# Kernel optimization log

Hardware: AMD Instinct MI355X
Metric: run time of the kernel (lower is better)

The kernel has to match this reference:

```python
import jax, jax.numpy as jnp
import numpy as np

B = 256       # decode batch
V = 50257     # per-model vocab size (GPT-2-class)
U = 65536     # union vocab size
M = 3         # number of ensembled models


def setup_inputs() -> dict:
    key = jax.random.key(0)
    ks = jax.random.split(key, 7)
    d = {}
    for i in range(M):
        d[f"logits{i}"] = jax.random.normal(ks[i], (B, V), dtype=jnp.float32)
    for i in range(M):
        # vocab_to_token_id mapping: model-local vocab index -> union vocab index
        d[f"map{i}"] = jax.random.randint(ks[M + i], (V,), 0, U, dtype=jnp.int32)
    d["weights"] = jnp.array([0.4, 0.35, 0.25], dtype=jnp.float32)
    return d


def reference(logits0, logits1, logits2, map0, map1, map2, weights):
    # union_probs[b, map_m[j]] += w_m * softmax(logits_m)[b, j]
    union = jnp.zeros((logits0.shape[0], U), dtype=logits0.dtype)
    for m, (lg, mp) in enumerate(zip((logits0, logits1, logits2),
                                     (map0, map1, map2))):
        p = jax.nn.softmax(lg, axis=-1)          # [B, V]
        union = union.at[:, mp].add(weights[m] * p)  # weighted scatter-add into [B, U]
    return union
```

## Files before the change

### kernel.cpp

```cpp
#include <hip/hip_runtime.h>

#define BB 256
#define VV 50257
#define UU 65536
#define MM 3
#define NT 1024

typedef float float4a __attribute__((ext_vector_type(4), aligned(4)));

#define WS_WINV   0
#define WS_HIST   3072
#define WS_OFF    7168
#define WS_CURSOR 11296
#define WS_SORTED 15392
#define WS_ET     618496
#define WS_NEED   77813248ull

__global__ __launch_bounds__(512) void row_sums_kernel(
    const float* __restrict__ l0, const float* __restrict__ l1,
    const float* __restrict__ l2, const float* __restrict__ weights,
    float* __restrict__ winv)
{
    const int bx = blockIdx.x;
    const int m  = bx >> 8;
    const int b  = bx & 255;
    const float* lg  = (m == 0) ? l0 : (m == 1) ? l1 : l2;
    const float* row = lg + (size_t)b * VV;
    const float4a* rowv = (const float4a*)row;

    const int nv4 = VV / 4;
    float partial = 0.0f;
    for (int i = threadIdx.x; i < nv4; i += 512) {
        float4a v = rowv[i];
        partial += __expf(v.x) + __expf(v.y) + __expf(v.z) + __expf(v.w);
    }
    if (threadIdx.x == 0) partial += __expf(row[VV - 1]);

    #pragma unroll
    for (int off = 32; off > 0; off >>= 1)
        partial += __shfl_down(partial, off, 64);

    __shared__ float smem[8];
    const int lane = threadIdx.x & 63;
    const int wv   = threadIdx.x >> 6;
    if (lane == 0) smem[wv] = partial;
    __syncthreads();
    if (threadIdx.x == 0) {
        float tot = 0.0f;
        #pragma unroll
        for (int w = 0; w < 8; ++w) tot += smem[w];
        winv[bx] = weights[m] / tot;
    }
}

__global__ __launch_bounds__(1024) void hist_count_kernel(
    const int* __restrict__ m0, const int* __restrict__ m1,
    const int* __restrict__ m2, int* __restrict__ hist)
{
    __shared__ int h[NT];
    for (int i = threadIdx.x; i < NT; i += 1024) h[i] = 0;
    __syncthreads();
    const int total = MM * VV;
    for (int idx = blockIdx.x * 1024 + threadIdx.x; idx < total;
         idx += gridDim.x * 1024) {
        const int m = idx / VV;
        const int j = idx - m * VV;
        const int* mp = (m == 0) ? m0 : (m == 1) ? m1 : m2;
        atomicAdd(&h[mp[j] >> 6], 1);
    }
    __syncthreads();
    for (int i = threadIdx.x; i < NT; i += 1024) atomicAdd(&hist[i], h[i]);
}

__global__ __launch_bounds__(1024) void prefix_kernel(
    const int* __restrict__ hist, int* __restrict__ off, int* __restrict__ cursor)
{
    __shared__ int s[NT];
    const int t = threadIdx.x;
    const int mine = hist[t];
    s[t] = mine;
    __syncthreads();
    for (int d = 1; d < NT; d <<= 1) {
        int v = (t >= d) ? s[t - d] : 0;
        __syncthreads();
        s[t] += v;
        __syncthreads();
    }
    const int excl = s[t] - mine;
    off[t] = excl;
    cursor[t] = excl;
    if (t == NT - 1) off[NT] = s[t];
}

__global__ __launch_bounds__(256) void sort_kernel(
    const int* __restrict__ m0, const int* __restrict__ m1,
    const int* __restrict__ m2, int* __restrict__ cursor,
    int* __restrict__ sorted)
{
    const int total = MM * VV;
    for (int idx = blockIdx.x * 256 + threadIdx.x; idx < total;
         idx += gridDim.x * 256) {
        const int m = idx / VV;
        const int j = idx - m * VV;
        const int* mp = (m == 0) ? m0 : (m == 1) ? m1 : m2;
        const int u = mp[j];
        const int pos = atomicAdd(&cursor[u >> 6], 1);
        sorted[pos] = (j << 8) | (m << 6) | (u & 63);
    }
}

__global__ __launch_bounds__(256) void transpose_exp_kernel(
    const float* __restrict__ l0, const float* __restrict__ l1,
    const float* __restrict__ l2, _Float16* __restrict__ ET)
{
    const int m  = blockIdx.z;
    const float* lg = (m == 0) ? l0 : (m == 1) ? l1 : l2;
    const int j0 = blockIdx.x * 64;
    const int b0 = blockIdx.y * 64;
    __shared__ float tile[64][65];
    const int lane = threadIdx.x & 63;
    const int sub  = threadIdx.x >> 6;

    const int j = j0 + lane;
    if (j < VV) {
        #pragma unroll
        for (int rr = 0; rr < 16; ++rr) {
            const int b = b0 + rr * 4 + sub;
            tile[lane][rr * 4 + sub] = __expf(lg[(size_t)b * VV + j]);
        }
    }
    __syncthreads();
    #pragma unroll
    for (int rr = 0; rr < 16; ++rr) {
        const int jj = rr * 4 + sub;
        const int jw = j0 + jj;
        if (jw < VV)
            ET[((size_t)m * VV + jw) * BB + b0 + lane] = (_Float16)tile[jj][lane];
    }
}

__global__ __launch_bounds__(256) void accumulate_kernel(
    const _Float16* __restrict__ ET, const int* __restrict__ sorted,
    const int* __restrict__ off, const float* __restrict__ winv,
    float* __restrict__ out)
{
    const int k = blockIdx.x;
    const int t = threadIdx.x;

    __shared__ float acc[64 * 256];
    for (int i = t; i < 64 * 256; i += 256) acc[i] = 0.0f;
    const float w0 = winv[0 * BB + t];
    const float w1 = winv[1 * BB + t];
    const float w2 = winv[2 * BB + t];
    __syncthreads();

    const int s = off[k], e = off[k + 1];
    #pragma unroll 4
    for (int i = s; i < e; ++i) {
        const int pack = sorted[i];
        const int ul = pack & 63;
        const int m  = (pack >> 6) & 3;
        const int j  = pack >> 8;
        const float ev = (float)ET[((size_t)m * VV + j) * BB + t];
        const float w  = (m == 0) ? w0 : (m == 1) ? w1 : w2;
        acc[ul * 256 + (t ^ (ul & 31))] += w * ev;
    }
    __syncthreads();

    const int u0 = k * 64;
    const int lane = t & 63, sub = t >> 6;
    #pragma unroll 4
    for (int c = 0; c < 64; ++c) {
        const int b = sub + c * 4;
        out[(size_t)b * UU + u0 + lane] = acc[lane * 256 + (b ^ (lane & 31))];
    }
}

#define FB_NBUCK 8
#define FB_BSZ   8192

__global__ __launch_bounds__(256) void fb_count_kernel(
    const int* __restrict__ m0, const int* __restrict__ m1,
    const int* __restrict__ m2, int* __restrict__ cnt)
{
    const int m = blockIdx.y;
    const int* mp = (m == 0) ? m0 : (m == 1) ? m1 : m2;
    __shared__ int hist[FB_NBUCK];
    if (threadIdx.x < FB_NBUCK) hist[threadIdx.x] = 0;
    __syncthreads();
    const int j = blockIdx.x * 256 + threadIdx.x;
    if (j < VV) atomicAdd(&hist[mp[j] >> 13], 1);
    __syncthreads();
    if (threadIdx.x < FB_NBUCK)
        atomicAdd(&cnt[m * FB_NBUCK + threadIdx.x], hist[threadIdx.x]);
}

__global__ void fb_prefix_kernel(const int* __restrict__ cnt,
                                 int* __restrict__ off, int* __restrict__ cursor)
{
    for (int m = 0; m < MM; ++m) {
        int acc = 0;
        for (int k = 0; k < FB_NBUCK; ++k) {
            off[m * (FB_NBUCK + 1) + k] = acc;
            cursor[m * FB_NBUCK + k]    = acc;
            acc += cnt[m * FB_NBUCK + k];
        }
        off[m * (FB_NBUCK + 1) + FB_NBUCK] = acc;
    }
}

__global__ __launch_bounds__(256) void fb_scatter_kernel(
    const int* __restrict__ m0, const int* __restrict__ m1,
    const int* __restrict__ m2, int* __restrict__ cursor,
    int* __restrict__ sorted)
{
    const int m = blockIdx.y;
    const int* mp = (m == 0) ? m0 : (m == 1) ? m1 : m2;
    int* srt = sorted + (size_t)m * VV;
    const int j = blockIdx.x * 256 + threadIdx.x;
    int u = 0, bucket = FB_NBUCK;
    if (j < VV) { u = mp[j]; bucket = u >> 13; }
    const int lane = threadIdx.x & 63;
    const unsigned long long lt = (1ull << lane) - 1ull;
    #pragma unroll
    for (int k = 0; k < FB_NBUCK; ++k) {
        unsigned long long mask = __ballot(bucket == k);
        if (mask) {
            int leader = __ffsll((long long)mask) - 1;
            int base = 0;
            if (lane == leader)
                base = atomicAdd(&cursor[m * FB_NBUCK + k], __popcll(mask));
            base = __shfl(base, leader, 64);
            if (bucket == k) {
                int pos = base + __popcll(mask & lt);
                srt[pos] = ((u & (FB_BSZ - 1)) << 16) | j;
            }
        }
    }
}

__global__ __launch_bounds__(512) void fb_accumulate_kernel(
    const float* __restrict__ l0, const float* __restrict__ l1,
    const float* __restrict__ l2,
    const int* __restrict__ sorted, const int* __restrict__ off,
    const float* __restrict__ winv, float* __restrict__ out)
{
    const int k = blockIdx.x;
    const int b = blockIdx.y;
    __shared__ float acc[FB_BSZ];
    for (int i = threadIdx.x; i < FB_BSZ; i += 512) acc[i] = 0.0f;
    __syncthreads();
    #pragma unroll
    for (int m = 0; m < MM; ++m) {
        const float* lg = (m == 0) ? l0 : (m == 1) ? l1 : l2;
        const float* row = lg + (size_t)b * VV;
        const int* srt = sorted + (size_t)m * VV;
        const float wv = winv[m * BB + b];
        const int s = off[m * (FB_NBUCK + 1) + k];
        const int e = off[m * (FB_NBUCK + 1) + k + 1];
        for (int i = s + threadIdx.x; i < e; i += 512) {
            const int pack = srt[i];
            atomicAdd(&acc[pack >> 16], wv * __expf(row[pack & 0xFFFF]));
        }
    }
    __syncthreads();
    float* orow = out + (size_t)b * UU + (size_t)k * FB_BSZ;
    for (int i = threadIdx.x; i < FB_BSZ; i += 512) orow[i] = acc[i];
}

extern "C" void kernel_launch(void* const* d_in, const int* in_sizes, int n_in,
                              void* d_out, int out_size, void* d_ws, size_t ws_size,
                              hipStream_t stream)
{
    const float* l0 = (const float*)d_in[0];
    const float* l1 = (const float*)d_in[1];
    const float* l2 = (const float*)d_in[2];
    const int*   m0 = (const int*)d_in[3];
    const int*   m1 = (const int*)d_in[4];
    const int*   m2 = (const int*)d_in[5];
    const float* w  = (const float*)d_in[6];
    float* out = (float*)d_out;
    char* ws = (char*)d_ws;

    if (ws_size >= WS_NEED) {
        float*    winv   = (float*)   (ws + WS_WINV);
        int*      hist   = (int*)     (ws + WS_HIST);
        int*      off    = (int*)     (ws + WS_OFF);
        int*      cursor = (int*)     (ws + WS_CURSOR);
        int*      sorted = (int*)     (ws + WS_SORTED);
        _Float16* ET     = (_Float16*)(ws + WS_ET);

        hipMemsetAsync(hist, 0, NT * sizeof(int), stream);

        row_sums_kernel<<<MM * BB, 512, 0, stream>>>(l0, l1, l2, w, winv);
        hist_count_kernel<<<64, 1024, 0, stream>>>(m0, m1, m2, hist);
        prefix_kernel<<<1, 1024, 0, stream>>>(hist, off, cursor);
        sort_kernel<<<256, 256, 0, stream>>>(m0, m1, m2, cursor, sorted);

        dim3 gtr((VV + 63) / 64, BB / 64, MM);
        transpose_exp_kernel<<<gtr, 256, 0, stream>>>(l0, l1, l2, ET);

        accumulate_kernel<<<NT, 256, 0, stream>>>(ET, sorted, off, winv, out);
    } else {
        float* winv   = (float*)(ws + 0);
        int*   cnt    = (int*)  (ws + 3072);
        int*   off    = (int*)  (ws + 3200);
        int*   cursor = (int*)  (ws + 3456);
        int*   sorted = (int*)  (ws + 3584);

        hipMemsetAsync(cnt, 0, MM * FB_NBUCK * sizeof(int), stream);
        row_sums_kernel<<<MM * BB, 512, 0, stream>>>(l0, l1, l2, w, winv);
        dim3 gmap((VV + 255) / 256, MM);
        fb_count_kernel<<<gmap, 256, 0, stream>>>(m0, m1, m2, cnt);
        fb_prefix_kernel<<<1, 1, 0, stream>>>(cnt, off, cursor);
        fb_scatter_kernel<<<gmap, 256, 0, stream>>>(m0, m1, m2, cursor, sorted);
        dim3 gacc(FB_NBUCK, BB);
        fb_accumulate_kernel<<<gacc, 512, 0, stream>>>(l0, l1, l2, sorted, off, winv, out);
    }
}
```

Baseline: 339.1 us.

## Fuse row sums into transpose-exp kernel and split accumulate across two warp groups

The separate row-sum pass over the logits is dropped. The transpose-exp kernel now loops over 8 column tiles per block and accumulates per-row partial sums of exp, which a small kernel reduces into the inverse weights. This removes one full read of the logits and one exp pass. The accumulate kernel now uses 512 threads, with two groups splitting the sorted entries and using shared-memory atomics, which raises parallelism at the cost of atomic overhead. The partials buffer reuses the sorted region, which is safe only because winv_kernel consumes the partials before sort_kernel overwrites them.

```diff
diff --git a/kernel.cpp b/kernel.cpp
--- a/kernel.cpp
+++ b/kernel.cpp
@@ -5,6 +5,8 @@
 #define UU 65536
 #define MM 3
 #define NT 1024
+#define NJT 786
+#define NJC 99
 
 typedef float float4a __attribute__((ext_vector_type(4), aligned(4)));
 
@@ -16,41 +18,66 @@
 #define WS_ET     618496
 #define WS_NEED   77813248ull
 
-__global__ __launch_bounds__(512) void row_sums_kernel(
+__global__ __launch_bounds__(256) void transpose_exp_sum_kernel(
     const float* __restrict__ l0, const float* __restrict__ l1,
-    const float* __restrict__ l2, const float* __restrict__ weights,
+    const float* __restrict__ l2, _Float16* __restrict__ ET,
+    float* __restrict__ partials)
+{
+    const int m  = blockIdx.z;
+    const float* lg = (m == 0) ? l0 : (m == 1) ? l1 : l2;
+    const int b0 = blockIdx.y * 64;
+    const int jc = blockIdx.x;
+    const int lane = threadIdx.x & 63;
+    const int sub  = threadIdx.x >> 6;
+
+    __shared__ float tile[64][65];
+    __shared__ float psum[4][64];
+    float fsum = 0.0f;
+
+    for (int tt = 0; tt < 8; ++tt) {
+        const int jt = jc * 8 + tt;
+        if (jt >= NJT) break;
+        const int j0 = jt * 64;
+        const int j  = j0 + lane;
+        if (j < VV) {
+            #pragma unroll
+            for (int rr = 0; rr < 16; ++rr) {
+                const int b = b0 + rr * 4 + sub;
+                tile[lane][rr * 4 + sub] = __expf(lg[(size_t)b * VV + j]);
+            }
+        }
+        __syncthreads();
+        #pragma unroll
+        for (int rr = 0; rr < 16; ++rr) {
+            const int jj = rr * 4 + sub;
+            const int jw = j0 + jj;
+            if (jw < VV) {
+                const float v = tile[jj][lane];
+                ET[((size_t)m * VV + jw) * BB + b0 + lane] = (_Float16)v;
+                fsum += v;
+            }
+        }
+        __syncthreads();
+    }
+    psum[sub][lane] = fsum;
+    __syncthreads();
+    if (threadIdx.x < 64) {
+        const float tot = psum[0][threadIdx.x] + psum[1][threadIdx.x]
+                        + psum[2][threadIdx.x] + psum[3][threadIdx.x];
+        partials[((m << 8) + b0 + threadIdx.x) * NJC + jc] = tot;
+    }
+}
+
+__global__ __launch_bounds__(64) void winv_kernel(
+    const float* __restrict__ partials, const float* __restrict__ weights,
     float* __restrict__ winv)
 {
-    const int bx = blockIdx.x;
-    const int m  = bx >> 8;
-    const int b  = bx & 255;
-    const float* lg  = (m == 0) ? l0 : (m == 1) ? l1 : l2;
-    const float* row = lg + (size_t)b * VV;
-    const float4a* rowv = (const float4a*)row;
-
-    const int nv4 = VV / 4;
-    float partial = 0.0f;
-    for (int i = threadIdx.x; i < nv4; i += 512) {
-        float4a v = rowv[i];
-        partial += __expf(v.x) + __expf(v.y) + __expf(v.z) + __expf(v.w);
-    }
-    if (threadIdx.x == 0) partial += __expf(row[VV - 1]);
-
-    #pragma unroll
-    for (int off = 32; off > 0; off >>= 1)
-        partial += __shfl_down(partial, off, 64);
-
-    __shared__ float smem[8];
-    const int lane = threadIdx.x & 63;
-    const int wv   = threadIdx.x >> 6;
-    if (lane == 0) smem[wv] = partial;
-    __syncthreads();
-    if (threadIdx.x == 0) {
-        float tot = 0.0f;
-        #pragma unroll
-        for (int w = 0; w < 8; ++w) tot += smem[w];
-        winv[bx] = weights[m] / tot;
-    }
+    const int row = blockIdx.x;
+    float p = 0.0f;
+    for (int i = threadIdx.x; i < NJC; i += 64) p += partials[row * NJC + i];
+    #pragma unroll
+    for (int o = 32; o > 0; o >>= 1) p += __shfl_down(p, o, 64);
+    if (threadIdx.x == 0) winv[row] = weights[row >> 8] / p;
 }
 
 __global__ __launch_bounds__(1024) void hist_count_kernel(
@@ -109,70 +136,73 @@
     }
 }
 
-__global__ __launch_bounds__(256) void transpose_exp_kernel(
-    const float* __restrict__ l0, const float* __restrict__ l1,
-    const float* __restrict__ l2, _Float16* __restrict__ ET)
-{
-    const int m  = blockIdx.z;
-    const float* lg = (m == 0) ? l0 : (m == 1) ? l1 : l2;
-    const int j0 = blockIdx.x * 64;
-    const int b0 = blockIdx.y * 64;
-    __shared__ float tile[64][65];
-    const int lane = threadIdx.x & 63;
-    const int sub  = threadIdx.x >> 6;
-
-    const int j = j0 + lane;
-    if (j < VV) {
-        #pragma unroll
-        for (int rr = 0; rr < 16; ++rr) {
-            const int b = b0 + rr * 4 + sub;
-            tile[lane][rr * 4 + sub] = __expf(lg[(size_t)b * VV + j]);
-        }
-    }
-    __syncthreads();
-    #pragma unroll
-    for (int rr = 0; rr < 16; ++rr) {
-        const int jj = rr * 4 + sub;
-        const int jw = j0 + jj;
-        if (jw < VV)
-            ET[((size_t)m * VV + jw) * BB + b0 + lane] = (_Float16)tile[jj][lane];
-    }
-}
-
-__global__ __launch_bounds__(256) void accumulate_kernel(
+__global__ __launch_bounds__(512) void accumulate_kernel(
     const _Float16* __restrict__ ET, const int* __restrict__ sorted,
     const int* __restrict__ off, const float* __restrict__ winv,
     float* __restrict__ out)
 {
     const int k = blockIdx.x;
     const int t = threadIdx.x;
+    const int b = t & 255;
+    const int g = t >> 8;
 
     __shared__ float acc[64 * 256];
-    for (int i = t; i < 64 * 256; i += 256) acc[i] = 0.0f;
-    const float w0 = winv[0 * BB + t];
-    const float w1 = winv[1 * BB + t];
-    const float w2 = winv[2 * BB + t];
+    for (int i = t; i < 64 * 256; i += 512) acc[i] = 0.0f;
+    const float w0 = winv[b], w1 = winv[256 + b], w2 = winv[512 + b];
     __syncthreads();
 
     const int s = off[k], e = off[k + 1];
     #pragma unroll 4
-    for (int i = s; i < e; ++i) {
+    for (int i = s + g; i < e; i += 2) {
         const int pack = sorted[i];
         const int ul = pack & 63;
         const int m  = (pack >> 6) & 3;
         const int j  = pack >> 8;
-        const float ev = (float)ET[((size_t)m * VV + j) * BB + t];
+        const float ev = (float)ET[((size_t)m * VV + j) * BB + b];
         const float w  = (m == 0) ? w0 : (m == 1) ? w1 : w2;
-        acc[ul * 256 + (t ^ (ul & 31))] += w * ev;
+        atomicAdd(&acc[ul * 256 + (b ^ (ul & 31))], w * ev);
     }
     __syncthreads();
 
     const int u0 = k * 64;
-    const int lane = t & 63, sub = t >> 6;
-    #pragma unroll 4
-    for (int c = 0; c < 64; ++c) {
-        const int b = sub + c * 4;
-        out[(size_t)b * UU + u0 + lane] = acc[lane * 256 + (b ^ (lane & 31))];
+    const int lane = t & 63, grp = t >> 6;
+    #pragma unroll
+    for (int c = 0; c < 32; ++c) {
+        const int bb = grp + c * 8;
+        out[(size_t)bb * UU + u0 + lane] = acc[lane * 256 + (bb ^ (lane & 31))];
+    }
+}
+
+__global__ __launch_bounds__(512) void row_sums_kernel(
+    const float* __restrict__ l0, const float* __restrict__ l1,
+    const float* __restrict__ l2, const float* __restrict__ weights,
+    float* __restrict__ winv)
+{
+    const int bx = blockIdx.x;
+    const int m  = bx >> 8;
+    const int b  = bx & 255;
+    const float* lg  = (m == 0) ? l0 : (m == 1) ? l1 : l2;
+    const float* row = lg + (size_t)b * VV;
+    const float4a* rowv = (const float4a*)row;
+    const int nv4 = VV / 4;
+    float partial = 0.0f;
+    for (int i = threadIdx.x; i < nv4; i += 512) {
+        float4a v = rowv[i];
+        partial += __expf(v.x) + __expf(v.y) + __expf(v.z) + __expf(v.w);
+    }
+    if (threadIdx.x == 0) partial += __expf(row[VV - 1]);
+    #pragma unroll
+    for (int o = 32; o > 0; o >>= 1) partial += __shfl_down(partial, o, 64);
+    __shared__ float smem[8];
+    const int lane = threadIdx.x & 63;
+    const int wv   = threadIdx.x >> 6;
+    if (lane == 0) smem[wv] = partial;
+    __syncthreads();
+    if (threadIdx.x == 0) {
+        float tot = 0.0f;
+        #pragma unroll
+        for (int w = 0; w < 8; ++w) tot += smem[w];
+        winv[bx] = weights[m] / tot;
     }
 }
 
@@ -283,24 +313,25 @@
     char* ws = (char*)d_ws;
 
     if (ws_size >= WS_NEED) {
-        float*    winv   = (float*)   (ws + WS_WINV);
-        int*      hist   = (int*)     (ws + WS_HIST);
-        int*      off    = (int*)     (ws + WS_OFF);
-        int*      cursor = (int*)     (ws + WS_CURSOR);
-        int*      sorted = (int*)     (ws + WS_SORTED);
-        _Float16* ET     = (_Float16*)(ws + WS_ET);
+        float*    winv     = (float*)   (ws + WS_WINV);
+        int*      hist     = (int*)     (ws + WS_HIST);
+        int*      off      = (int*)     (ws + WS_OFF);
+        int*      cursor   = (int*)     (ws + WS_CURSOR);
+        int*      sorted   = (int*)     (ws + WS_SORTED);
+        float*    partials = (float*)   (ws + WS_SORTED);
+        _Float16* ET       = (_Float16*)(ws + WS_ET);
 
         hipMemsetAsync(hist, 0, NT * sizeof(int), stream);
 
-        row_sums_kernel<<<MM * BB, 512, 0, stream>>>(l0, l1, l2, w, winv);
+        dim3 gtr(NJC, BB / 64, MM);
+        transpose_exp_sum_kernel<<<gtr, 256, 0, stream>>>(l0, l1, l2, ET, partials);
+        winv_kernel<<<MM * BB, 64, 0, stream>>>(partials, w, winv);
+
         hist_count_kernel<<<64, 1024, 0, stream>>>(m0, m1, m2, hist);
         prefix_kernel<<<1, 1024, 0, stream>>>(hist, off, cursor);
         sort_kernel<<<256, 256, 0, stream>>>(m0, m1, m2, cursor, sorted);
 
-        dim3 gtr((VV + 63) / 64, BB / 64, MM);
-        transpose_exp_kernel<<<gtr, 256, 0, stream>>>(l0, l1, l2, ET);
-
-        accumulate_kernel<<<NT, 256, 0, stream>>>(ET, sorted, off, winv, out);
+        accumulate_kernel<<<NT, 512, 0, stream>>>(ET, sorted, off, winv, out);
     } else {
         float* winv   = (float*)(ws + 0);
         int*   cnt    = (int*)  (ws + 3072);
```

After: 502.1 us. +48.1%, slower.
